# Kernel optimization log

Hardware: AMD Instinct MI355X
Metric: run time of the kernel (lower is better)

## Reference

```python
import jax, jax.numpy as jnp
import numpy as np

N_ENT = 30000
ALL_REL = 221
N_DIM = 32
L = 2
EVAL_REL = 86
B = 16
E = 120000


def setup_inputs() -> dict:
    key = jax.random.key(0)
    ks = jax.random.split(key, 16)
    d = N_DIM
    inp = {
        'head': jax.random.randint(ks[0], (B,), 0, N_ENT),
        'tail': jax.random.randint(ks[1], (B,), 0, N_ENT),
        'edge_heads': jax.random.randint(ks[2], (E,), 0, N_ENT),
        'edge_tails': jax.random.randint(ks[3], (E,), 0, N_ENT),
        'edge_rels': jax.random.randint(ks[4], (E,), 0, ALL_REL),
        'edge_weight': jnp.ones((E,), jnp.float32),
        # learned params (xavier-ish scale)
        'ent_emb': jax.random.normal(ks[5], (N_ENT, d), jnp.float32) * 0.05,
        'rel_embs': jax.random.normal(ks[6], (L, ALL_REL, d), jnp.float32) * 0.1,
        'Wlin': jax.random.normal(ks[7], (L, d, d), jnp.float32) * (1.0 / np.sqrt(d)),
        'blin': jnp.zeros((L, d), jnp.float32),
        'Wrel': jax.random.normal(ks[8], (L, 2 * d, 5), jnp.float32) * 0.1,
        'brel': jnp.zeros((L, 5), jnp.float32),
        'Watt': jax.random.normal(ks[9], (L, 5, ALL_REL), jnp.float32) * 0.3,
        'batt': jnp.zeros((L, ALL_REL), jnp.float32),
        'Wr': jax.random.normal(ks[10], (4 * d, EVAL_REL), jnp.float32) * 0.1,
        'br': jnp.zeros((EVAL_REL,), jnp.float32),
    }
    return inp


def _propagate(init_emb, init_idx, ht_embed, rel_embs, Wlin, blin, Wrel, brel,
               Watt, batt, edge_weight, eh, et, er):
    # init_emb: (B, d); hiddens: (n_ent, B, d)
    Bn, d = init_emb.shape
    hid = jnp.zeros((N_ENT, Bn, d), init_emb.dtype)
    hid = hid.at[init_idx, jnp.arange(Bn)].set(init_emb)
    for l in range(L):
        # per-sample relation attention weights: (B, all_rel)
        relw = jax.nn.sigmoid(jax.nn.relu(ht_embed @ Wrel[l] + brel[l]) @ Watt[l] + batt[l])
        # generalized rspmm: out[t] += w * (relw[:, r] * rel_emb[r]) * hid[h]
        msg = hid[eh] * (relw.T[er][:, :, None] * rel_embs[l][er][:, None, :])  # (E, B, d)
        msg = msg * edge_weight[:, None, None]
        hid = jax.ops.segment_sum(msg, et, num_segments=N_ENT)  # (n_ent, B, d)
        hid = jax.nn.relu(hid @ Wlin[l] + blin[l])
    return hid


def reference(head, tail, edge_heads, edge_tails, edge_rels, edge_weight,
              ent_emb, rel_embs, Wlin, blin, Wrel, brel, Watt, batt, Wr, br):
    head_embed = ent_emb[head]  # (B, d)
    tail_embed = ent_emb[tail]
    ht_embed = jnp.concatenate([head_embed, tail_embed], axis=-1)  # (B, 2d)

    # head -> tail propagation
    hid = _propagate(head_embed, head, ht_embed, rel_embs, Wlin, blin, Wrel, brel,
                     Watt, batt, edge_weight, edge_heads, edge_tails, edge_rels)
    tail_hid = hid[tail, jnp.arange(tail.shape[0])]  # (B, d)

    # tail -> head propagation (same KG, same layers, per original code)
    hid = _propagate(tail_embed, tail, ht_embed, rel_embs, Wlin, blin, Wrel, brel,
                     Watt, batt, edge_weight, edge_heads, edge_tails, edge_rels)
    head_hid = hid[head, jnp.arange(head.shape[0])]

    embeddings = jnp.concatenate([head_embed, tail_embed, head_hid, tail_hid], axis=1)
    return embeddings @ Wr + br  # (B, eval_rel)
```

## Files before the change

### kernel.cpp

```cpp
#include <hip/hip_runtime.h>
#include <math.h>

#define N_ENTC 30000
#define ALL_RELC 221
#define NDIM 32
#define EVAL_RELC 86
#define BB 16
#define NE 120000
#define ROW 512
#define NSCAN 120
#define EPB 1000
#define MW 938


__global__ __launch_bounds__(512) void k_scan(
    const int* __restrict__ head, const int* __restrict__ tail,
    const int* __restrict__ eh, const int* __restrict__ et,
    const int* __restrict__ er, const float* __restrict__ ew,
    const float* __restrict__ ent_emb,
    const float* __restrict__ Wrel, const float* __restrict__ brel,
    const float* __restrict__ Watt, const float* __restrict__ batt,
    int4* __restrict__ recs, int* __restrict__ counts,
    float* __restrict__ relwG, float* __restrict__ hidB,
    float* __restrict__ qaccB)
{
    __shared__ unsigned mH[MW], mT[MW];
    __shared__ int s_src[32];
    __shared__ int s_cnt[4];
    __shared__ float s_ht[BB * 64];
    __shared__ float s_h5[BB * 5];
    const int t = threadIdx.x, bid = blockIdx.x;

    if (t < 32) s_src[t] = (t < BB) ? head[t] : tail[t - BB];
    for (int i = t; i < MW; i += 512) { mH[i] = 0u; mT[i] = 0u; }
    if (t < 4) s_cnt[t] = 0;
    __syncthreads();
    if (t < BB) {
        int h = s_src[t], q = s_src[BB + t];
        atomicOr(&mH[h >> 5], 1u << (h & 31));
        atomicOr(&mT[q >> 5], 1u << (q & 31));
    }
    __syncthreads();

    const int e0 = bid * EPB;
    const int4* eh4 = (const int4*)(eh + e0);
    const int4* et4 = (const int4*)(et + e0);
    for (int p = t; p < EPB / 4; p += 512) {
        int4 h4 = eh4[p], t4 = et4[p];
        int hv[4] = {h4.x, h4.y, h4.z, h4.w};
        int tv[4] = {t4.x, t4.y, t4.z, t4.w};
#pragma unroll
        for (int c = 0; c < 4; c++) {
            int e = e0 + 4 * p + c, h = hv[c], tt = tv[c];
            bool hH = (mH[h >> 5] >> (h & 31)) & 1u;
            bool hT = (mT[h >> 5] >> (h & 31)) & 1u;
            bool tT = (mT[tt >> 5] >> (tt & 31)) & 1u;
            bool tH = (mH[tt >> 5] >> (tt & 31)) & 1u;
            if (!(hH | hT | tT | tH)) continue;
            int r = er[e];
            int wb = __float_as_int(ew[e]);
            if (hH) {
                unsigned m = 0;
#pragma unroll
                for (int b = 0; b < BB; b++) m |= (s_src[b] == h) ? (1u << b) : 0u;
                int pos = atomicAdd(&s_cnt[0], 1);
                recs[(size_t)bid * EPB + pos] = make_int4(tt, r | (int)(m << 8), wb, h);
            }
            if (hT) {
                unsigned m = 0;
#pragma unroll
                for (int b = 0; b < BB; b++) m |= (s_src[BB + b] == h) ? (1u << b) : 0u;
                int pos = atomicAdd(&s_cnt[1], 1);
                recs[(size_t)NE + bid * EPB + pos] = make_int4(tt, r | (int)(m << 8), wb, h);
            }
            if (tT) {
                unsigned m = 0;
#pragma unroll
                for (int b = 0; b < BB; b++) m |= (s_src[BB + b] == tt) ? (1u << b) : 0u;
                int canon = __ffs(m) - 1;
                int pos = atomicAdd(&s_cnt[2], 1);
                recs[(size_t)2 * NE + bid * EPB + pos] = make_int4(h, r | (canon << 8), wb, tt);
            }
            if (tH) {
                unsigned m = 0;
#pragma unroll
                for (int b = 0; b < BB; b++) m |= (s_src[b] == tt) ? (1u << b) : 0u;
                int canon = __ffs(m) - 1;
                int pos = atomicAdd(&s_cnt[3], 1);
                recs[(size_t)3 * NE + bid * EPB + pos] = make_int4(h, r | (canon << 8), wb, tt);
            }
        }
    }
    __syncthreads();
    if (t < 4) counts[bid * 4 + t] = s_cnt[t];

    {
        const int wid8 = t >> 6, lane = t & 63;
        float4 z = make_float4(0.f, 0.f, 0.f, 0.f);
        for (int li = 2; li < 4; li++) {
            int c = s_cnt[li];
            float* hb = hidB + (size_t)(li - 2) * N_ENTC * ROW;
            for (int j = wid8; j < c; j += 8) {
                int row = recs[(size_t)li * NE + bid * EPB + j].x;
                float4* p = (float4*)(hb + (size_t)row * ROW);
                p[lane] = z;
                p[lane + 64] = z;
            }
        }
    }

    if (bid == 1) {
        for (int i = t; i < 2 * BB * ROW; i += 512) qaccB[i] = 0.f;
    }
    if (bid == 0) {
        for (int i = t; i < BB * NDIM; i += 512) {
            int b = i >> 5, k = i & 31;
            s_ht[b * 64 + k] = ent_emb[(size_t)s_src[b] * NDIM + k];
            s_ht[b * 64 + 32 + k] = ent_emb[(size_t)s_src[BB + b] * NDIM + k];
        }
        __syncthreads();
        for (int l = 0; l < 2; l++) {
            for (int i = t; i < BB * 5; i += 512) {
                int b = i / 5, j = i % 5;
                float s = brel[l * 5 + j];
                for (int k = 0; k < 64; k++)
                    s += s_ht[b * 64 + k] * Wrel[l * 320 + k * 5 + j];
                s_h5[i] = fmaxf(s, 0.f);
            }
            __syncthreads();
            for (int i = t; i < BB * ALL_RELC; i += 512) {
                int b = i / ALL_RELC, r = i % ALL_RELC;
                float s = batt[l * ALL_RELC + r];
                for (int j = 0; j < 5; j++)
                    s += s_h5[b * 5 + j] * Watt[l * 5 * ALL_RELC + j * ALL_RELC + r];
                relwG[l * BB * ALL_RELC + i] = 1.0f / (1.0f + expf(-s));
            }
            __syncthreads();
        }
    }
}

__global__ __launch_bounds__(256) void k_msg1(
    const int* __restrict__ head, const int* __restrict__ tail,
    const float* __restrict__ ent_emb, const float* __restrict__ rel_embs,
    const int4* __restrict__ recs, const int* __restrict__ counts,
    const float* __restrict__ relwG, float* __restrict__ hidB)
{
    __shared__ int s_src[32];
    const int t = threadIdx.x, bid = blockIdx.x;
    int4 c4 = ((const int4*)counts)[bid];
    if ((c4.x | c4.y) == 0) return;
    if (t < 32) s_src[t] = (t < BB) ? head[t] : tail[t - BB];
    __syncthreads();
    const int wid = t >> 6, lane = t & 63;
    const float4* rv0 = (const float4*)rel_embs;
    for (int d = 0; d < 2; d++) {
        int c = d ? c4.y : c4.x;
        const int4* R = recs + (size_t)d * NE + (size_t)bid * EPB;
        float* hb = hidB + (size_t)d * N_ENTC * ROW;
        for (int j = wid; j < c; j += 4) {
            int4 rec = R[j];
            int tt = rec.x, r = rec.y & 255;
            unsigned msk = ((unsigned)rec.y) >> 8;
            float w = __int_as_float(rec.z);
            float* drow = hb + (size_t)tt * ROW;
#pragma unroll
            for (int ii = 0; ii < 2; ii++) {
                int i4 = lane + 64 * ii, b = i4 >> 3, kq = i4 & 7;
                if (!((msk >> b) & 1u)) continue;
                float cf = relwG[b * ALL_RELC + r] * w;
                float4 sv = ((const float4*)(ent_emb + (size_t)s_src[d * BB + b] * NDIM))[kq];
                float4 rr = rv0[r * 8 + kq];
                atomicAdd(drow + i4 * 4 + 0, sv.x * cf * rr.x);
                atomicAdd(drow + i4 * 4 + 1, sv.y * cf * rr.y);
                atomicAdd(drow + i4 * 4 + 2, sv.z * cf * rr.z);
                atomicAdd(drow + i4 * 4 + 3, sv.w * cf * rr.w);
            }
        }
    }
}

__global__ __launch_bounds__(256) void k_lin1(
    const int4* __restrict__ recs, const int* __restrict__ counts,
    const float* __restrict__ Wlin, const float* __restrict__ blin,
    const float* __restrict__ hidB, float* __restrict__ hidC)
{
    __shared__ float sW[NDIM * NDIM];
    __shared__ float sb[NDIM];
    const int t = threadIdx.x, bid = blockIdx.x;
    int4 c4 = ((const int4*)counts)[bid];
    if ((c4.z | c4.w) == 0) return;
    for (int i = t; i < NDIM * NDIM; i += 256) sW[i] = Wlin[i];
    if (t < NDIM) sb[t] = blin[t];
    __syncthreads();
    const int wid = t >> 6, lane = t & 63;
    int b = lane >> 2, j0 = (lane & 3) * 8;
    for (int d = 0; d < 2; d++) {
        int c = d ? c4.w : c4.z;
        const int4* R = recs + (size_t)(2 + d) * NE + (size_t)bid * EPB;
        const float* hb = hidB + (size_t)d * N_ENTC * ROW;
        float* hc = hidC + (size_t)d * N_ENTC * ROW;
        for (int j = wid; j < c; j += 4) {
            int row = R[j].x;
            const float4* src = (const float4*)(hb + (size_t)row * ROW + b * NDIM);
            float h[NDIM];
#pragma unroll
            for (int q = 0; q < 8; q++) {
                float4 v = src[q];
                h[q * 4 + 0] = v.x; h[q * 4 + 1] = v.y;
                h[q * 4 + 2] = v.z; h[q * 4 + 3] = v.w;
            }
            float acc[8];
#pragma unroll
            for (int jj = 0; jj < 8; jj++) acc[jj] = sb[j0 + jj];
#pragma unroll
            for (int k = 0; k < NDIM; k++) {
                float4 w0 = *(const float4*)&sW[k * NDIM + j0];
                float4 w1 = *(const float4*)&sW[k * NDIM + j0 + 4];
                float hk = h[k];
                acc[0] += hk * w0.x; acc[1] += hk * w0.y;
                acc[2] += hk * w0.z; acc[3] += hk * w0.w;
                acc[4] += hk * w1.x; acc[5] += hk * w1.y;
                acc[6] += hk * w1.z; acc[7] += hk * w1.w;
            }
            float* dst = hc + (size_t)row * ROW + b * NDIM;
            float4 o0, o1;
            o0.x = fmaxf(acc[0], 0.f); o0.y = fmaxf(acc[1], 0.f);
            o0.z = fmaxf(acc[2], 0.f); o0.w = fmaxf(acc[3], 0.f);
            o1.x = fmaxf(acc[4], 0.f); o1.y = fmaxf(acc[5], 0.f);
            o1.z = fmaxf(acc[6], 0.f); o1.w = fmaxf(acc[7], 0.f);
            *(float4*)(dst + j0) = o0;
            *(float4*)(dst + j0 + 4) = o1;
        }
    }
}

__global__ __launch_bounds__(256) void k_msg2(
    const int4* __restrict__ recs, const int* __restrict__ counts,
    const float* __restrict__ rel_embs, const float* __restrict__ relwG,
    const float* __restrict__ hidC, float* __restrict__ qaccB)
{
    const int t = threadIdx.x, bid = blockIdx.x;
    int4 c4 = ((const int4*)counts)[bid];
    if ((c4.z | c4.w) == 0) return;
    const int wid = t >> 6, lane = t & 63;
    const float4* rv1 = (const float4*)(rel_embs + (size_t)ALL_RELC * NDIM);
    for (int d = 0; d < 2; d++) {
        int c = d ? c4.w : c4.z;
        const int4* R = recs + (size_t)(2 + d) * NE + (size_t)bid * EPB;
        const float* hc = hidC + (size_t)d * N_ENTC * ROW;
        float* qa = qaccB + (size_t)d * BB * ROW;
        for (int j = wid; j < c; j += 4) {
            int4 rec = R[j];
            int h = rec.x, r = rec.y & 255, canon = (rec.y >> 8) & 15;
            float w = __int_as_float(rec.z);
            const float4* srow = (const float4*)(hc + (size_t)h * ROW);
            float* drow = qa + canon * ROW;
#pragma unroll
            for (int ii = 0; ii < 2; ii++) {
                int i4 = lane + 64 * ii, b = i4 >> 3, kq = i4 & 7;
                float cf = relwG[BB * ALL_RELC + b * ALL_RELC + r] * w;
                float4 s = srow[i4];
                float4 rr = rv1[r * 8 + kq];
                atomicAdd(drow + i4 * 4 + 0, s.x * cf * rr.x);
                atomicAdd(drow + i4 * 4 + 1, s.y * cf * rr.y);
                atomicAdd(drow + i4 * 4 + 2, s.z * cf * rr.z);
                atomicAdd(drow + i4 * 4 + 3, s.w * cf * rr.w);
            }
        }
    }
}

__global__ __launch_bounds__(512) void k_fin(
    const int* __restrict__ head, const int* __restrict__ tail,
    const float* __restrict__ ent_emb, const float* __restrict__ Wlin,
    const float* __restrict__ blin, const float* __restrict__ Wr,
    const float* __restrict__ br, const float* __restrict__ qaccB,
    float* __restrict__ out)
{
    __shared__ float sx[BB * 128];
    __shared__ float sW[NDIM * NDIM];
    __shared__ float sb[NDIM];
    __shared__ int s_src[32];
    __shared__ int s_canon[2][BB];
    const int t = threadIdx.x;

    if (t < 32) s_src[t] = (t < BB) ? head[t] : tail[t - BB];
    for (int i = t; i < NDIM * NDIM; i += 512) sW[i] = Wlin[NDIM * NDIM + i];
    if (t < NDIM) sb[t] = blin[NDIM + t];
    __syncthreads();
    if (t < 2 * BB) {
        int d = t >> 4, b = t & 15;
        int q = s_src[(1 - d) * BB + b];
        int c = 0;
        for (int bb = 0; bb < BB; bb++)
            if (s_src[(1 - d) * BB + bb] == q) { c = bb; break; }
        s_canon[d][b] = c;
    }
    {
        int b = t >> 5, k = t & 31;
        sx[b * 128 + k] = ent_emb[(size_t)s_src[b] * NDIM + k];
        sx[b * 128 + 32 + k] = ent_emb[(size_t)s_src[BB + b] * NDIM + k];
    }
    __syncthreads();
    for (int d = 0; d < 2; d++) {
        int b = t >> 5, j = t & 31;
        const float* hrow = qaccB + (size_t)d * BB * ROW + s_canon[d][b] * ROW + b * NDIM;
        float s = sb[j];
        for (int k = 0; k < NDIM; k++)
            s += hrow[k] * sW[k * NDIM + j];
        sx[b * 128 + (d == 0 ? 96 : 64) + j] = fmaxf(s, 0.f);
    }
    __syncthreads();
    for (int o = t; o < BB * EVAL_RELC; o += 512) {
        int b = o / EVAL_RELC, r = o % EVAL_RELC;
        float s = br[r];
        for (int k = 0; k < 128; k++)
            s += sx[b * 128 + k] * Wr[k * EVAL_RELC + r];
        out[o] = s;
    }
}

extern "C" void kernel_launch(void* const* d_in, const int* in_sizes, int n_in,
                              void* d_out, int out_size, void* d_ws,
                              size_t ws_size, hipStream_t stream)
{
    const int* head = (const int*)d_in[0];
    const int* tail = (const int*)d_in[1];
    const int* eh = (const int*)d_in[2];
    const int* et = (const int*)d_in[3];
    const int* er = (const int*)d_in[4];
    const float* ew = (const float*)d_in[5];
    const float* ent_emb = (const float*)d_in[6];
    const float* rel_embs = (const float*)d_in[7];
    const float* Wlin = (const float*)d_in[8];
    const float* blin = (const float*)d_in[9];
    const float* Wrel = (const float*)d_in[10];
    const float* brel = (const float*)d_in[11];
    const float* Watt = (const float*)d_in[12];
    const float* batt = (const float*)d_in[13];
    const float* Wr = (const float*)d_in[14];
    const float* br = (const float*)d_in[15];
    float* out = (float*)d_out;
    float* ws = (float*)d_ws;

    float* hidB = ws;
    float* hidC = hidB + (size_t)2 * N_ENTC * ROW;
    int4* recs = (int4*)(hidC + (size_t)2 * N_ENTC * ROW);
    int* counts = (int*)(recs + (size_t)4 * NE);
    float* relwG = (float*)(counts + 4 * NSCAN);
    float* qaccB = relwG + 7072;

    k_scan<<<NSCAN, 512, 0, stream>>>(head, tail, eh, et, er, ew, ent_emb,
                                      Wrel, brel, Watt, batt,
                                      recs, counts, relwG, hidB, qaccB);
    k_msg1<<<NSCAN, 256, 0, stream>>>(head, tail, ent_emb, rel_embs,
                                      recs, counts, relwG, hidB);
    k_lin1<<<NSCAN, 256, 0, stream>>>(recs, counts, Wlin, blin, hidB, hidC);
    k_msg2<<<NSCAN, 256, 0, stream>>>(recs, counts, rel_embs, relwG,
                                      hidC, qaccB);
    k_fin<<<1, 512, 0, stream>>>(head, tail, ent_emb, Wlin, blin, Wr, br,
                                 qaccB, out);
}
```

Measured before the change: 119.9 us.

## Fuse layer-1 linear, layer-2 messages and final head into one kernel

Merges k_lin1, k_msg2 and k_fin into a single kernel. The linear+ReLU output for each row is kept in a per-wave shared-memory tile and scattered straight into the accumulators, so the hidC global buffer is no longer written and re-read. A last-block ticket counter with release/acquire fences lets the final block run the output head without a separate launch. This cuts two kernel launches and a global round trip, in exchange for a serialized tail on one block and the ticket synchronization.

```diff
diff --git a/kernel.cpp b/kernel.cpp
--- a/kernel.cpp
+++ b/kernel.cpp
@@ -22,7 +22,7 @@
     const float* __restrict__ Watt, const float* __restrict__ batt,
     int4* __restrict__ recs, int* __restrict__ counts,
     float* __restrict__ relwG, float* __restrict__ hidB,
-    float* __restrict__ qaccB)
+    float* __restrict__ qaccB, unsigned* __restrict__ ticket)
 {
     __shared__ unsigned mH[MW], mT[MW];
     __shared__ int s_src[32];
@@ -111,6 +111,7 @@
 
     if (bid == 1) {
         for (int i = t; i < 2 * BB * ROW; i += 512) qaccB[i] = 0.f;
+        if (t == 0) *ticket = 0u;
     }
     if (bid == 0) {
         for (int i = t; i < BB * NDIM; i += 512) {
@@ -180,114 +181,101 @@
     }
 }
 
-__global__ __launch_bounds__(256) void k_lin1(
+__global__ __launch_bounds__(256) void k_tail2(
+    const int* __restrict__ head, const int* __restrict__ tail,
+    const float* __restrict__ ent_emb, const float* __restrict__ rel_embs,
+    const float* __restrict__ Wlin, const float* __restrict__ blin,
+    const float* __restrict__ Wr, const float* __restrict__ br,
     const int4* __restrict__ recs, const int* __restrict__ counts,
-    const float* __restrict__ Wlin, const float* __restrict__ blin,
-    const float* __restrict__ hidB, float* __restrict__ hidC)
+    const float* __restrict__ relwG, const float* __restrict__ hidB,
+    float* __restrict__ qaccB, unsigned* __restrict__ ticket,
+    float* __restrict__ out)
 {
     __shared__ float sW[NDIM * NDIM];
     __shared__ float sb[NDIM];
-    const int t = threadIdx.x, bid = blockIdx.x;
-    int4 c4 = ((const int4*)counts)[bid];
-    if ((c4.z | c4.w) == 0) return;
-    for (int i = t; i < NDIM * NDIM; i += 256) sW[i] = Wlin[i];
-    if (t < NDIM) sb[t] = blin[t];
-    __syncthreads();
-    const int wid = t >> 6, lane = t & 63;
-    int b = lane >> 2, j0 = (lane & 3) * 8;
-    for (int d = 0; d < 2; d++) {
-        int c = d ? c4.w : c4.z;
-        const int4* R = recs + (size_t)(2 + d) * NE + (size_t)bid * EPB;
-        const float* hb = hidB + (size_t)d * N_ENTC * ROW;
-        float* hc = hidC + (size_t)d * N_ENTC * ROW;
-        for (int j = wid; j < c; j += 4) {
-            int row = R[j].x;
-            const float4* src = (const float4*)(hb + (size_t)row * ROW + b * NDIM);
-            float h[NDIM];
-#pragma unroll
-            for (int q = 0; q < 8; q++) {
-                float4 v = src[q];
-                h[q * 4 + 0] = v.x; h[q * 4 + 1] = v.y;
-                h[q * 4 + 2] = v.z; h[q * 4 + 3] = v.w;
-            }
-            float acc[8];
-#pragma unroll
-            for (int jj = 0; jj < 8; jj++) acc[jj] = sb[j0 + jj];
-#pragma unroll
-            for (int k = 0; k < NDIM; k++) {
-                float4 w0 = *(const float4*)&sW[k * NDIM + j0];
-                float4 w1 = *(const float4*)&sW[k * NDIM + j0 + 4];
-                float hk = h[k];
-                acc[0] += hk * w0.x; acc[1] += hk * w0.y;
-                acc[2] += hk * w0.z; acc[3] += hk * w0.w;
-                acc[4] += hk * w1.x; acc[5] += hk * w1.y;
-                acc[6] += hk * w1.z; acc[7] += hk * w1.w;
-            }
-            float* dst = hc + (size_t)row * ROW + b * NDIM;
-            float4 o0, o1;
-            o0.x = fmaxf(acc[0], 0.f); o0.y = fmaxf(acc[1], 0.f);
-            o0.z = fmaxf(acc[2], 0.f); o0.w = fmaxf(acc[3], 0.f);
-            o1.x = fmaxf(acc[4], 0.f); o1.y = fmaxf(acc[5], 0.f);
-            o1.z = fmaxf(acc[6], 0.f); o1.w = fmaxf(acc[7], 0.f);
-            *(float4*)(dst + j0) = o0;
-            *(float4*)(dst + j0 + 4) = o1;
-        }
-    }
-}
-
-__global__ __launch_bounds__(256) void k_msg2(
-    const int4* __restrict__ recs, const int* __restrict__ counts,
-    const float* __restrict__ rel_embs, const float* __restrict__ relwG,
-    const float* __restrict__ hidC, float* __restrict__ qaccB)
-{
-    const int t = threadIdx.x, bid = blockIdx.x;
-    int4 c4 = ((const int4*)counts)[bid];
-    if ((c4.z | c4.w) == 0) return;
-    const int wid = t >> 6, lane = t & 63;
-    const float4* rv1 = (const float4*)(rel_embs + (size_t)ALL_RELC * NDIM);
-    for (int d = 0; d < 2; d++) {
-        int c = d ? c4.w : c4.z;
-        const int4* R = recs + (size_t)(2 + d) * NE + (size_t)bid * EPB;
-        const float* hc = hidC + (size_t)d * N_ENTC * ROW;
-        float* qa = qaccB + (size_t)d * BB * ROW;
-        for (int j = wid; j < c; j += 4) {
-            int4 rec = R[j];
-            int h = rec.x, r = rec.y & 255, canon = (rec.y >> 8) & 15;
-            float w = __int_as_float(rec.z);
-            const float4* srow = (const float4*)(hc + (size_t)h * ROW);
-            float* drow = qa + canon * ROW;
-#pragma unroll
-            for (int ii = 0; ii < 2; ii++) {
-                int i4 = lane + 64 * ii, b = i4 >> 3, kq = i4 & 7;
-                float cf = relwG[BB * ALL_RELC + b * ALL_RELC + r] * w;
-                float4 s = srow[i4];
-                float4 rr = rv1[r * 8 + kq];
-                atomicAdd(drow + i4 * 4 + 0, s.x * cf * rr.x);
-                atomicAdd(drow + i4 * 4 + 1, s.y * cf * rr.y);
-                atomicAdd(drow + i4 * 4 + 2, s.z * cf * rr.z);
-                atomicAdd(drow + i4 * 4 + 3, s.w * cf * rr.w);
-            }
-        }
-    }
-}
-
-__global__ __launch_bounds__(512) void k_fin(
-    const int* __restrict__ head, const int* __restrict__ tail,
-    const float* __restrict__ ent_emb, const float* __restrict__ Wlin,
-    const float* __restrict__ blin, const float* __restrict__ Wr,
-    const float* __restrict__ br, const float* __restrict__ qaccB,
-    float* __restrict__ out)
-{
-    __shared__ float sx[BB * 128];
-    __shared__ float sW[NDIM * NDIM];
-    __shared__ float sb[NDIM];
+    __shared__ float s_tile[4][512];
     __shared__ int s_src[32];
     __shared__ int s_canon[2][BB];
-    const int t = threadIdx.x;
-
+    __shared__ unsigned s_last;
+    const int t = threadIdx.x, bid = blockIdx.x;
+    const int wid = t >> 6, lane = t & 63;
+
+    int4 c4 = ((const int4*)counts)[bid];
+    if (c4.z | c4.w) {
+        for (int i = t; i < NDIM * NDIM; i += 256) sW[i] = Wlin[i];
+        if (t < NDIM) sb[t] = blin[t];
+        __syncthreads();
+        const int b4 = lane >> 2, j0 = (lane & 3) * 8;
+        const float* rw1 = relwG + BB * ALL_RELC;
+        const float4* rv1 = (const float4*)(rel_embs + (size_t)ALL_RELC * NDIM);
+        float* tw = &s_tile[wid][0];
+        for (int d = 0; d < 2; d++) {
+            int c = d ? c4.w : c4.z;
+            const int4* R = recs + (size_t)(2 + d) * NE + (size_t)bid * EPB;
+            const float* hb = hidB + (size_t)d * N_ENTC * ROW;
+            float* qa = qaccB + (size_t)d * BB * ROW;
+            for (int j = wid; j < c; j += 4) {
+                int4 rec = R[j];
+                int row = rec.x, r = rec.y & 255, canon = (rec.y >> 8) & 15;
+                float w = __int_as_float(rec.z);
+                const float4* src = (const float4*)(hb + (size_t)row * ROW + b4 * NDIM);
+                float h[NDIM];
+#pragma unroll
+                for (int q = 0; q < 8; q++) {
+                    float4 v = src[q];
+                    h[q * 4 + 0] = v.x; h[q * 4 + 1] = v.y;
+                    h[q * 4 + 2] = v.z; h[q * 4 + 3] = v.w;
+                }
+                float acc[8];
+#pragma unroll
+                for (int jj = 0; jj < 8; jj++) acc[jj] = sb[j0 + jj];
+#pragma unroll
+                for (int k = 0; k < NDIM; k++) {
+                    float4 w0 = *(const float4*)&sW[k * NDIM + j0];
+                    float4 w1 = *(const float4*)&sW[k * NDIM + j0 + 4];
+                    float hk = h[k];
+                    acc[0] += hk * w0.x; acc[1] += hk * w0.y;
+                    acc[2] += hk * w0.z; acc[3] += hk * w0.w;
+                    acc[4] += hk * w1.x; acc[5] += hk * w1.y;
+                    acc[6] += hk * w1.z; acc[7] += hk * w1.w;
+                }
+                float4 o0, o1;
+                o0.x = fmaxf(acc[0], 0.f); o0.y = fmaxf(acc[1], 0.f);
+                o0.z = fmaxf(acc[2], 0.f); o0.w = fmaxf(acc[3], 0.f);
+                o1.x = fmaxf(acc[4], 0.f); o1.y = fmaxf(acc[5], 0.f);
+                o1.z = fmaxf(acc[6], 0.f); o1.w = fmaxf(acc[7], 0.f);
+                *(float4*)&tw[b4 * NDIM + j0] = o0;
+                *(float4*)&tw[b4 * NDIM + j0 + 4] = o1;
+                float* drow = qa + canon * ROW;
+#pragma unroll
+                for (int ii = 0; ii < 2; ii++) {
+                    int i4 = lane + 64 * ii, b = i4 >> 3, kq = i4 & 7;
+                    float cf = rw1[b * ALL_RELC + r] * w;
+                    float4 s = *(const float4*)&tw[b * NDIM + kq * 4];
+                    float4 rr = rv1[r * 8 + kq];
+                    atomicAdd(drow + i4 * 4 + 0, s.x * cf * rr.x);
+                    atomicAdd(drow + i4 * 4 + 1, s.y * cf * rr.y);
+                    atomicAdd(drow + i4 * 4 + 2, s.z * cf * rr.z);
+                    atomicAdd(drow + i4 * 4 + 3, s.w * cf * rr.w);
+                }
+            }
+        }
+    }
+    __syncthreads();
+    if (t == 0) {
+        __builtin_amdgcn_fence(__ATOMIC_RELEASE, "agent");
+        s_last = __hip_atomic_fetch_add(ticket, 1u, __ATOMIC_RELAXED,
+                                        __HIP_MEMORY_SCOPE_AGENT);
+    }
+    __syncthreads();
+    if (s_last != NSCAN - 1) return;
+    if (t == 0) __builtin_amdgcn_fence(__ATOMIC_ACQUIRE, "agent");
+    __syncthreads();
+
+    float* sx = &s_tile[0][0];
+    for (int i = t; i < NDIM * NDIM; i += 256) sW[i] = Wlin[NDIM * NDIM + i];
+    if (t < NDIM) sb[t] = blin[NDIM + t];
     if (t < 32) s_src[t] = (t < BB) ? head[t] : tail[t - BB];
-    for (int i = t; i < NDIM * NDIM; i += 512) sW[i] = Wlin[NDIM * NDIM + i];
-    if (t < NDIM) sb[t] = blin[NDIM + t];
     __syncthreads();
     if (t < 2 * BB) {
         int d = t >> 4, b = t & 15;
@@ -297,22 +285,25 @@
             if (s_src[(1 - d) * BB + bb] == q) { c = bb; break; }
         s_canon[d][b] = c;
     }
-    {
-        int b = t >> 5, k = t & 31;
+    for (int i = t; i < BB * NDIM; i += 256) {
+        int b = i >> 5, k = i & 31;
         sx[b * 128 + k] = ent_emb[(size_t)s_src[b] * NDIM + k];
         sx[b * 128 + 32 + k] = ent_emb[(size_t)s_src[BB + b] * NDIM + k];
     }
     __syncthreads();
     for (int d = 0; d < 2; d++) {
-        int b = t >> 5, j = t & 31;
-        const float* hrow = qaccB + (size_t)d * BB * ROW + s_canon[d][b] * ROW + b * NDIM;
-        float s = sb[j];
-        for (int k = 0; k < NDIM; k++)
-            s += hrow[k] * sW[k * NDIM + j];
-        sx[b * 128 + (d == 0 ? 96 : 64) + j] = fmaxf(s, 0.f);
-    }
-    __syncthreads();
-    for (int o = t; o < BB * EVAL_RELC; o += 512) {
+        for (int i = t; i < 512; i += 256) {
+            int b = i >> 5, j = i & 31;
+            const float* hrow = qaccB + (size_t)d * BB * ROW
+                                + s_canon[d][b] * ROW + b * NDIM;
+            float s = sb[j];
+            for (int k = 0; k < NDIM; k++)
+                s += hrow[k] * sW[k * NDIM + j];
+            sx[b * 128 + (d == 0 ? 96 : 64) + j] = fmaxf(s, 0.f);
+        }
+    }
+    __syncthreads();
+    for (int o = t; o < BB * EVAL_RELC; o += 256) {
         int b = o / EVAL_RELC, r = o % EVAL_RELC;
         float s = br[r];
         for (int k = 0; k < 128; k++)
@@ -345,20 +336,18 @@
     float* ws = (float*)d_ws;
 
     float* hidB = ws;
-    float* hidC = hidB + (size_t)2 * N_ENTC * ROW;
-    int4* recs = (int4*)(hidC + (size_t)2 * N_ENTC * ROW);
+    int4* recs = (int4*)(hidB + (size_t)2 * N_ENTC * ROW);
     int* counts = (int*)(recs + (size_t)4 * NE);
     float* relwG = (float*)(counts + 4 * NSCAN);
     float* qaccB = relwG + 7072;
+    unsigned* ticket = (unsigned*)(qaccB + 2 * BB * ROW);
 
     k_scan<<<NSCAN, 512, 0, stream>>>(head, tail, eh, et, er, ew, ent_emb,
                                       Wrel, brel, Watt, batt,
-                                      recs, counts, relwG, hidB, qaccB);
+                                      recs, counts, relwG, hidB, qaccB, ticket);
     k_msg1<<<NSCAN, 256, 0, stream>>>(head, tail, ent_emb, rel_embs,
                                       recs, counts, relwG, hidB);
-    k_lin1<<<NSCAN, 256, 0, stream>>>(recs, counts, Wlin, blin, hidB, hidC);
-    k_msg2<<<NSCAN, 256, 0, stream>>>(recs, counts, rel_embs, relwG,
-                                      hidC, qaccB);
-    k_fin<<<1, 512, 0, stream>>>(head, tail, ent_emb, Wlin, blin, Wr, br,
-                                 qaccB, out);
+    k_tail2<<<NSCAN, 256, 0, stream>>>(head, tail, ent_emb, rel_embs,
+                                       Wlin, blin, Wr, br, recs, counts,
+                                       relwG, hidB, qaccB, ticket, out);
 }
```

After: 132.0 us. +10.0%, slower.
